# Kernel optimization log

Measured on AMD Instinct MI355X. Metric: run time of the kernel, lower is better.

## Reference

```python
import jax, jax.numpy as jnp
import numpy as np
import math

B, T, DIM = 4, 4096, 1024
HID = int(DIM * 1.5)  # 1536
K = 4                  # conv kernel size
S = 16                 # num_slots
D = 384                # slot_dim


def setup_inputs() -> dict:
    key = jax.random.key(0)
    ks = jax.random.split(key, 16)
    inp = {
        "x": jax.random.normal(ks[0], (B, T, DIM), jnp.float32),
        "input_w": jax.random.normal(ks[1], (2 * HID, DIM), jnp.float32) * DIM ** -0.5,
        "conv_w": jax.random.normal(ks[2], (HID, K), jnp.float32) * K ** -0.5,
        "conv_b": jnp.zeros((HID,), jnp.float32),
        "gates_w": jax.random.normal(ks[3], (2 * HID, HID), jnp.float32) * HID ** -0.5,
        "gates_b": jnp.zeros((2 * HID,), jnp.float32),
        "forget_base": jnp.linspace(-4.323, -9.0, HID).astype(jnp.float32),
        "output_w": jax.random.normal(ks[4], (DIM, HID), jnp.float32) * HID ** -0.5,
        "memory_slots": jax.random.normal(ks[5], (S, D), jnp.float32) * 0.02,
        "wq_w": jax.random.normal(ks[6], (D, D), jnp.float32) * 0.02,
        "wk_w": jax.random.normal(ks[7], (D, HID), jnp.float32) * 0.02,
        "wv_w": jax.random.normal(ks[8], (D, HID), jnp.float32) * 0.02,
        "wg_w": jax.random.normal(ks[9], (1, HID), jnp.float32) * 0.02,
        "rq_w": jax.random.normal(ks[10], (D, HID), jnp.float32) * 0.02,
        "rk_w": jax.random.normal(ks[11], (D, D), jnp.float32) * 0.02,
        "rv_w": jax.random.normal(ks[12], (HID, D), jnp.float32) * 0.02,
    }
    return inp


def _causal_dwconv(x, w, b):
    # x: [B,T,H], w: [H,K], b: [H]; torch Conv1d(padding=K-1) then [:, :T] == causal
    xp = jnp.pad(x, ((0, 0), (K - 1, 0), (0, 0)))
    taps = jnp.stack([xp[:, j:j + T, :] for j in range(K)], axis=-1)  # [B,T,H,K]
    return jnp.einsum('bthk,hk->bth', taps, w) + b


def _scan(alpha, x):
    # h_t = alpha_t * h_{t-1} + x_t, elementwise over channels; along axis 1 (time)
    def combine(c1, c2):
        a1, b1 = c1
        a2, b2 = c2
        return a1 * a2, a2 * b1 + b2
    return jax.lax.associative_scan(combine, (alpha, x), axis=1)[1]


def reference(x, input_w, conv_w, conv_b, gates_w, gates_b, forget_base, output_w,
              memory_slots, wq_w, wk_w, wv_w, wg_w, rq_w, rk_w, rv_w):
    L = T // S  # segment length
    proj = x @ input_w.T                       # [B,T,2H]
    gate, xh = proj[..., :HID], proj[..., HID:]
    xh = _causal_dwconv(xh, conv_w, conv_b)    # [B,T,H]
    g = xh @ gates_w.T + gates_b               # [B,T,2H]
    forget, inp = g[..., :HID], g[..., HID:]
    alpha = jnp.exp(-8.0 * jax.nn.softplus(forget_base) * jax.nn.sigmoid(forget))
    xh = jnp.sqrt(1.0 - alpha ** 2 + 1e-6) * jax.nn.sigmoid(inp) * xh
    h = _scan(alpha, xh)                       # [B,T,H]
    xh = gate * jax.nn.sigmoid(gate) * xh      # silu-gated

    # ---- write_memory(xh) ----
    xseg = xh.reshape(B, S, L, HID)
    q = memory_slots @ wq_w.T                  # [S,D]
    kmat = jnp.einsum('bslh,dh->bsld', xseg, wk_w)
    vmat = jnp.einsum('bslh,dh->bsld', xseg, wv_w)
    qk = jnp.einsum('sd,bsld->bsl', q, kmat) / math.sqrt(D)
    attn = jax.nn.softmax(qk, axis=-1)
    mem = jnp.einsum('bsl,bsld->bsd', attn, vmat)  # [B,S,D]

    # ---- read_memory(gelu(xh)*h, mem) ----
    xr = jax.nn.gelu(xh, approximate=False) * h    # [B,T,H]
    rq = xr @ rq_w.T                               # [B,T,D]
    rk = mem @ rk_w.T                              # [B,S,D]
    rv = mem @ rv_w.T                              # [B,S,H]
    qk2 = jnp.einsum('btd,bsd->bts', rq, rk) / math.sqrt(D)
    seg = jnp.arange(T) // L
    mask = seg[:, None] <= jnp.arange(S)[None, :]  # [T,S]
    qk2 = jnp.where(mask[None], qk2, -jnp.inf)
    attn2 = jax.nn.softmax(qk2, axis=-1)
    out = jnp.einsum('bts,bsh->bth', attn2, rv)
    out = jax.nn.sigmoid(xr @ wg_w.T) * out        # write_gate on xr
    return out @ output_w.T                        # [B,T,DIM]
```

## Files before the change

kernel.cpp:

```cpp
#include <hip/hip_runtime.h>
#include <math.h>

#define BB 4
#define TT 4096
#define DIMW 1024
#define HID 1536
#define HID2 3072
#define KC 4
#define SSEG 16
#define LSEG 256
#define DD 384
#define NCH 64
#define CHL 64
#define TH  ((size_t)TT*(size_t)HID)

typedef _Float16 h8 __attribute__((ext_vector_type(8)));
typedef float f4 __attribute__((ext_vector_type(4)));

#define RSCL 4.8828125e-4f

__device__ __forceinline__ void hsplit(float a, _Float16& h0, _Float16& h1)
{
    _Float16 t = (_Float16)a;
    float tf = (float)t;
    if (fabsf(tf) < 6.103515625e-05f) { t = (_Float16)0.f; tf = 0.f; }
    h0 = t;
    h1 = (_Float16)((a - tf) * 2048.0f);
}

__device__ __forceinline__ void gl_lds16(const _Float16* g, _Float16* l)
{
    __builtin_amdgcn_global_load_lds(
        (const __attribute__((address_space(1))) unsigned int*)g,
        (__attribute__((address_space(3))) unsigned int*)l,
        16, 0, 0);
}

__global__ __launch_bounds__(256) void split2t(const float* __restrict__ src,
                                               _Float16* __restrict__ dst,
                                               int R, int Kd, size_t ps)
{
    __shared__ float tile[64][65];
    const int tid = threadIdx.x;
    const int bx = blockIdx.x;
    const int by = blockIdx.y;
    {
        const int lr = tid >> 2;
        const int lc = (tid & 3) * 16;
        const float* s = src + (size_t)(by * 64 + lr) * Kd + bx * 64 + lc;
#pragma unroll
        for (int e = 0; e < 16; e++) tile[lr][lc + e] = s[e];
    }
    __syncthreads();
    const int c = tid >> 5;
    const int r0 = tid & 31;
#pragma unroll
    for (int rr = 0; rr < 2; rr++) {
        const int r = r0 + rr * 32;
        h8 h0v, h1v;
#pragma unroll
        for (int e = 0; e < 8; e++) {
            _Float16 a0, a1;
            hsplit(tile[r][c * 8 + e], a0, a1);
            h0v[e] = a0; h1v[e] = a1;
        }
        const size_t didx = ((size_t)(bx * 8 + c) * R + by * 64 + r) * 8;
        *(h8*)(dst + didx) = h0v;
        *(h8*)(dst + ps + didx) = h1v;
    }
}

__global__ __launch_bounds__(256) void catkv_kernel(const float* __restrict__ wk,
                                                    const float* __restrict__ wv,
                                                    float* __restrict__ wkv)
{
    const int half = DD * HID;
    int i = blockIdx.x * 256 + threadIdx.x;
    if (i < half) wkv[i] = wk[i];
    else if (i < 2 * half) wkv[i] = wv[i - half];
}

template<int MODE, int TM, int TN, int WRN, int WCN>
__global__ __launch_bounds__(WRN * WCN * 64, 2) void gemm_mfma(
    const _Float16* __restrict__ Ap, size_t aps,
    const _Float16* __restrict__ Wp, size_t wps,
    float* __restrict__ C0, float* __restrict__ C1,
    const float* __restrict__ X,
    _Float16* __restrict__ OP, size_t ops,
    int M, int Nout, int Kd)
{
    constexpr int NWAVE = WRN * WCN;
    constexpr int WTM = TM / WRN, WTN = TN / WCN;
    constexpr int MI = WTM / 16, NI = WTN / 16;
    constexpr int API = TM / 16;
    constexpr int BPI = TN / 16;
    constexpr int ATOT = 2 * API;
    constexpr int NISS = ATOT + 2 * BPI;
    static_assert(NISS % NWAVE == 0, "issue count must divide waves");
    constexpr bool DUAL = (MI * NI <= 16);

    __shared__ _Float16 Als[2][2][TM * 32];
    __shared__ _Float16 Bls[2][2][TN * 32];

    const int tid = threadIdx.x;
    const int lane = tid & 63;
    const int wv = tid >> 6;
    const int wr = wv / WCN, wc = wv % WCN;
    const int lr = lane & 15, lg = lane >> 4;

    int bx = blockIdx.x, by = blockIdx.y;
    {
        const int gx = gridDim.x;
        const int nwg = gx * gridDim.y;
        if ((nwg & 7) == 0) {
            int wg = by * gx + bx;
            wg = (wg & 7) * (nwg >> 3) + (wg >> 3);
            bx = wg % gx; by = wg / gx;
        }
    }
    const int m0 = bx * TM, n0 = by * TN;

    f4 acc1[MI][NI], acc2[MI][NI];
#pragma unroll
    for (int i = 0; i < MI; i++)
#pragma unroll
        for (int j = 0; j < NI; j++) {
            acc1[i][j] = (f4){0.f, 0.f, 0.f, 0.f};
            if constexpr (DUAL) acc2[i][j] = (f4){0.f, 0.f, 0.f, 0.f};
        }

    auto stage = [&](int kq0, int buf) {
#pragma unroll
        for (int j = 0; j < NISS / NWAVE; j++) {
            const int i = j * NWAVE + wv;
            if (i < ATOT) {
                const int pl = i / API, s = i - pl * API;
                const int kc = (s * 64) / TM, r0 = (s * 64) % TM;
                const _Float16* g = Ap + pl * aps
                    + ((size_t)(kq0 + kc) * M + m0 + r0) * 8 + lane * 8;
                gl_lds16(g, &Als[buf][pl][(kc * TM + r0) * 8]);
            } else {
                const int jj = i - ATOT;
                const int pl = jj / BPI, s = jj - pl * BPI;
                const int kc = (s * 64) / TN, r0 = (s * 64) % TN;
                const _Float16* g = Wp + pl * wps
                    + ((size_t)(kq0 + kc) * Nout + n0 + r0) * 8 + lane * 8;
                gl_lds16(g, &Bls[buf][pl][(kc * TN + r0) * 8]);
            }
        }
    };

    stage(0, 0);
    __syncthreads();

    const int NS = Kd / 32;
    for (int t = 0; t < NS; t++) {
        const int buf = t & 1;
        if (t + 1 < NS) stage((t + 1) * 4, buf ^ 1);

        h8 af0[MI], af1[MI];
#pragma unroll
        for (int mi = 0; mi < MI; mi++) {
            const int arow = wr * WTM + mi * 16 + lr;
            af0[mi] = *(const h8*)&Als[buf][0][(lg * TM + arow) * 8];
            af1[mi] = *(const h8*)&Als[buf][1][(lg * TM + arow) * 8];
        }
#pragma unroll
        for (int ni = 0; ni < NI; ni++) {
            const int brow = wc * WTN + ni * 16 + lr;
            h8 b0 = *(const h8*)&Bls[buf][0][(lg * TN + brow) * 8];
            h8 b1 = *(const h8*)&Bls[buf][1][(lg * TN + brow) * 8];
#pragma unroll
            for (int mi = 0; mi < MI; mi++) {
                acc1[mi][ni] = __builtin_amdgcn_mfma_f32_16x16x32_f16(af0[mi], b0, acc1[mi][ni], 0, 0, 0);
                if constexpr (DUAL) {
                    acc2[mi][ni] = __builtin_amdgcn_mfma_f32_16x16x32_f16(af1[mi], b0, acc2[mi][ni], 0, 0, 0);
                    acc2[mi][ni] = __builtin_amdgcn_mfma_f32_16x16x32_f16(af0[mi], b1, acc2[mi][ni], 0, 0, 0);
                } else {
                    f4 tmp = (f4){0.f, 0.f, 0.f, 0.f};
                    tmp = __builtin_amdgcn_mfma_f32_16x16x32_f16(af1[mi], b0, tmp, 0, 0, 0);
                    tmp = __builtin_amdgcn_mfma_f32_16x16x32_f16(af0[mi], b1, tmp, 0, 0, 0);
                    acc1[mi][ni] = acc1[mi][ni] + tmp * RSCL;
                }
            }
        }
        __syncthreads();
    }

#pragma unroll
    for (int mi = 0; mi < MI; mi++) {
#pragma unroll
        for (int ni = 0; ni < NI; ni++) {
#pragma unroll
            for (int r = 0; r < 4; r++) {
                float v;
                if constexpr (DUAL) v = acc1[mi][ni][r] + acc2[mi][ni][r] * RSCL;
                else                v = acc1[mi][ni][r];
                const int m = m0 + wr * WTM + mi * 16 + lg * 4 + r;
                const int n = n0 + wc * WTN + ni * 16 + lr;
                if constexpr (MODE == 1) {
                    if (n < HID) C0[(size_t)m * HID + n] = v;
                    else         C1[(size_t)m * HID + (n - HID)] = v;
                } else if constexpr (MODE == 2) {
                    double g = (double)v;
                    float fv = (float)((g / (1.0 + exp(-g))) * (double)X[(size_t)m * Nout + n]);
                    C0[(size_t)m * Nout + n] = fv;
                    _Float16 a0, a1;
                    hsplit(fv, a0, a1);
                    const size_t didx = ((size_t)(n >> 3) * M + m) * 8 + (n & 7);
                    OP[didx] = a0;
                    OP[ops + didx] = a1;
                } else {
                    C0[(size_t)m * Nout + n] = v;
                }
            }
        }
    }
}

template<int MODE, int TM, int TN>
__global__ __launch_bounds__(256) void gemm32(const float* __restrict__ A,
                                              const float* __restrict__ W,
                                              float* __restrict__ C0,
                                              float* __restrict__ C1,
                                              const float* __restrict__ X,
                                              int M, int Nout, int Kd)
{
    constexpr int GM = TM / 64;
    constexpr int GN = TN / 64;
    constexpr int AF4 = TM * 4;
    constexpr int WF4 = TN * 4;
    constexpr int ALOOP = (AF4 + 255) / 256;
    constexpr int WLOOP = (WF4 + 255) / 256;

    __shared__ float As[16][TM];
    __shared__ float Bs[16][TN];

    const int tid = threadIdx.x;
    const int m0 = blockIdx.x * TM;
    const int n0 = blockIdx.y * TN;
    const int tx = tid & 15, ty = tid >> 4;

    float acc[GM * 4][GN * 4];
#pragma unroll
    for (int i = 0; i < GM * 4; i++)
#pragma unroll
        for (int j = 0; j < GN * 4; j++) acc[i][j] = 0.0f;

    float4 aReg[ALOOP], wReg[WLOOP];

    auto issueLoads = [&](int k0) {
#pragma unroll
        for (int u = 0; u < ALOOP; u++) {
            const int idx = tid + u * 256;
            float4 v = make_float4(0.f, 0.f, 0.f, 0.f);
            if (idx < AF4) {
                const int row = idx >> 2, kq = (idx & 3) * 4;
                const long ar = (long)(m0 + row);
                if (ar < M) v = *(const float4*)(A + ar * (long)Kd + (k0 + kq));
            }
            aReg[u] = v;
        }
#pragma unroll
        for (int u = 0; u < WLOOP; u++) {
            const int idx = tid + u * 256;
            float4 v = make_float4(0.f, 0.f, 0.f, 0.f);
            if (idx < WF4) {
                const int row = idx >> 2, kq = (idx & 3) * 4;
                const long wr = (long)(n0 + row);
                v = *(const float4*)(W + wr * (long)Kd + (k0 + kq));
            }
            wReg[u] = v;
        }
    };
    auto writeLDS = [&]() {
#pragma unroll
        for (int u = 0; u < ALOOP; u++) {
            const int idx = tid + u * 256;
            if (idx < AF4) {
                const int row = idx >> 2, kq = (idx & 3) * 4;
                As[kq + 0][row] = aReg[u].x;
                As[kq + 1][row] = aReg[u].y;
                As[kq + 2][row] = aReg[u].z;
                As[kq + 3][row] = aReg[u].w;
            }
        }
#pragma unroll
        for (int u = 0; u < WLOOP; u++) {
            const int idx = tid + u * 256;
            if (idx < WF4) {
                const int row = idx >> 2, kq = (idx & 3) * 4;
                Bs[kq + 0][row] = wReg[u].x;
                Bs[kq + 1][row] = wReg[u].y;
                Bs[kq + 2][row] = wReg[u].z;
                Bs[kq + 3][row] = wReg[u].w;
            }
        }
    };

    issueLoads(0);
    writeLDS();
    __syncthreads();

    const int NT = Kd / 16;
    for (int t = 0; t < NT; t++) {
        if (t + 1 < NT) issueLoads((t + 1) * 16);
#pragma unroll
        for (int k = 0; k < 16; k++) {
            float a[GM * 4], b[GN * 4];
#pragma unroll
            for (int g = 0; g < GM; g++) {
                const float4 t4 = *(const float4*)&As[k][g * 64 + ty * 4];
                a[g * 4 + 0] = t4.x; a[g * 4 + 1] = t4.y;
                a[g * 4 + 2] = t4.z; a[g * 4 + 3] = t4.w;
            }
#pragma unroll
            for (int g = 0; g < GN; g++) {
                const float4 t4 = *(const float4*)&Bs[k][g * 64 + tx * 4];
                b[g * 4 + 0] = t4.x; b[g * 4 + 1] = t4.y;
                b[g * 4 + 2] = t4.z; b[g * 4 + 3] = t4.w;
            }
#pragma unroll
            for (int i = 0; i < GM * 4; i++)
#pragma unroll
                for (int j = 0; j < GN * 4; j++) acc[i][j] += a[i] * b[j];
        }
        __syncthreads();
        if (t + 1 < NT) {
            writeLDS();
            __syncthreads();
        }
    }

#pragma unroll
    for (int i = 0; i < GM * 4; i++) {
        const int m = m0 + (i >> 2) * 64 + ty * 4 + (i & 3);
        if (m >= M) continue;
#pragma unroll
        for (int j = 0; j < GN * 4; j++) {
            const int n = n0 + (j >> 2) * 64 + tx * 4 + (j & 3);
            if (n >= Nout) continue;
            C0[(long)m * Nout + n] = acc[i][j];
        }
    }
}

__global__ __launch_bounds__(256) void spb_kernel(const float* __restrict__ fb,
                                                  double* __restrict__ spb)
{
    int h = blockIdx.x * 256 + threadIdx.x;
    if (h < HID) {
        double xv = (double)fb[h];
        spb[h] = log1p(exp(xv));
    }
}

__global__ __launch_bounds__(256) void conv_kernel(const float* __restrict__ xin,
                                                   const float* __restrict__ cw,
                                                   const float* __restrict__ cb,
                                                   float* __restrict__ outp,
                                                   _Float16* __restrict__ outP,
                                                   size_t ps)
{
    size_t i = (size_t)blockIdx.x * 256 + threadIdx.x;
    if (i >= TH) return;
    int h = (int)(i % HID);
    int t = (int)(i / HID);
    double acc = (double)cb[h];
#pragma unroll
    for (int j = 0; j < KC; j++) {
        int tt = t - (KC - 1) + j;
        if (tt >= 0) acc += (double)cw[h * KC + j] * (double)xin[(size_t)tt * HID + h];
    }
    float fv = (float)acc;
    outp[i] = fv;
    _Float16 a0, a1;
    hsplit(fv, a0, a1);
    const size_t didx = ((size_t)(h >> 3) * TT + t) * 8 + (h & 7);
    outP[didx] = a0;
    outP[ps + didx] = a1;
}

__global__ __launch_bounds__(256) void alpha_xh2_kernel(float* __restrict__ fg,
                                                        float* __restrict__ ip,
                                                        const float* __restrict__ xh1,
                                                        const double* __restrict__ spb,
                                                        const float* __restrict__ gb)
{
    size_t i = (size_t)blockIdx.x * 256 + threadIdx.x;
    if (i >= TH) return;
    int h = (int)(i % HID);
    double f  = (double)fg[i] + (double)gb[h];
    double g2 = (double)ip[i] + (double)gb[HID + h];
    double sigf = 1.0 / (1.0 + exp(-f));
    double alpha = exp(-8.0 * spb[h] * sigf);
    double s2 = sqrt(1.0 - alpha * alpha + 1e-6);
    double sigi = 1.0 / (1.0 + exp(-g2));
    double x1 = (double)xh1[i];
    fg[i] = (float)alpha;
    ip[i] = (float)(s2 * sigi * x1);
}

__global__ __launch_bounds__(256) void scan1_kernel(const float* __restrict__ alpha,
                                                    const float* __restrict__ xh2,
                                                    double* __restrict__ cA,
                                                    double* __restrict__ cB)
{
    int idx = blockIdx.x * 256 + threadIdx.x;
    if (idx >= NCH * HID) return;
    int h = idx % HID;
    int c = idx / HID;
    size_t base = (size_t)c * CHL * HID + h;
    double aP = 1.0, bV = 0.0;
    for (int i = 0; i < CHL; i++) {
        double a  = (double)alpha[base + (size_t)i * HID];
        double xv = (double)xh2 [base + (size_t)i * HID];
        bV = a * bV + xv;
        aP *= a;
    }
    size_t o = (size_t)c * HID + h;
    cA[o] = aP;
    cB[o] = bV;
}

__global__ __launch_bounds__(256) void scan2_kernel(const double* __restrict__ cA,
                                                    const double* __restrict__ cB,
                                                    double* __restrict__ cH0)
{
    int h = blockIdx.x * 256 + threadIdx.x;
    if (h >= HID) return;
    double carry = 0.0;
    for (int c = 0; c < NCH; c++) {
        size_t o = (size_t)c * HID + h;
        cH0[o] = carry;
        carry = cA[o] * carry + cB[o];
    }
}

__global__ __launch_bounds__(256) void scan3_kernel(const float* __restrict__ alpha,
                                                    const float* __restrict__ xh2,
                                                    const double* __restrict__ cH0,
                                                    float* __restrict__ hout)
{
    int idx = blockIdx.x * 256 + threadIdx.x;
    if (idx >= NCH * HID) return;
    int h = idx % HID;
    int c = idx / HID;
    size_t base = (size_t)c * CHL * HID + h;
    double hv = cH0[(size_t)c * HID + h];
    for (int i = 0; i < CHL; i++) {
        double a  = (double)alpha[base + (size_t)i * HID];
        double xv = (double)xh2 [base + (size_t)i * HID];
        hv = a * hv + xv;
        hout[base + (size_t)i * HID] = (float)hv;
    }
}

__global__ __launch_bounds__(256) void gelu_mul_kernel(float* __restrict__ xh3,
                                                       const float* __restrict__ hbuf,
                                                       _Float16* __restrict__ outP,
                                                       size_t ps)
{
    size_t i = (size_t)blockIdx.x * 256 + threadIdx.x;
    if (i >= TH) return;
    int h = (int)(i % HID);
    int t = (int)(i / HID);
    double x3 = (double)xh3[i];
    double ge = 0.5 * x3 * (1.0 + erf(x3 * 0.70710678118654752440));
    float fv = (float)(ge * (double)hbuf[i]);
    xh3[i] = fv;
    _Float16 a0, a1;
    hsplit(fv, a0, a1);
    const size_t didx = ((size_t)(h >> 3) * TT + t) * 8 + (h & 7);
    outP[didx] = a0;
    outP[ps + didx] = a1;
}

__global__ __launch_bounds__(256) void attn1_kernel(const float* __restrict__ kv,
                                                    const float* __restrict__ qbuf,
                                                    float* __restrict__ mem)
{
    const int s = blockIdx.x;
    const int l = threadIdx.x;
    const size_t row = (size_t)s * LSEG + l;
    const float* kr = kv + row * (2 * DD);
    const float* qs = qbuf + (size_t)s * DD;
    double acc = 0.0;
    for (int d = 0; d < DD; d++) acc += (double)qs[d] * (double)kr[d];
    double qk = acc / sqrt((double)DD);
    __shared__ double r1[256];
    __shared__ double sw[256];
    r1[l] = qk; __syncthreads();
    for (int off = 128; off > 0; off >>= 1) {
        if (l < off) r1[l] = fmax(r1[l], r1[l + off]);
        __syncthreads();
    }
    double m = r1[0]; __syncthreads();
    double e = exp(qk - m);
    r1[l] = e; __syncthreads();
    for (int off = 128; off > 0; off >>= 1) {
        if (l < off) r1[l] += r1[l + off];
        __syncthreads();
    }
    double denom = r1[0];
    sw[l] = e / denom; __syncthreads();
    const size_t vbase = (size_t)s * LSEG * (2 * DD) + DD;
    for (int d = l; d < DD; d += 256) {
        double a2 = 0.0;
        for (int ll = 0; ll < LSEG; ll++)
            a2 += sw[ll] * (double)kv[vbase + (size_t)ll * (2 * DD) + d];
        mem[(size_t)s * DD + d] = (float)a2;
    }
}

__global__ __launch_bounds__(256) void attn2_kernel(const float* __restrict__ rq,
                                                    const float* __restrict__ rk,
                                                    const float* __restrict__ rv,
                                                    const float* __restrict__ xr,
                                                    const float* __restrict__ wg,
                                                    _Float16* __restrict__ outP,
                                                    size_t ps)
{
    const int t = blockIdx.x;
    const int sigma = t >> 8;
    const int tid = threadIdx.x;
    __shared__ double sqk[16];
    __shared__ double red[256];
    __shared__ double sw[16];
    __shared__ double sgate;

    const float* rqn = rq + (size_t)t * DD;
    {
        int s = tid >> 4, j = tid & 15;
        const float* rks = rk + (size_t)s * DD;
        double part = 0.0;
        for (int d = j; d < DD; d += 16) part += (double)rqn[d] * (double)rks[d];
#pragma unroll
        for (int off = 8; off > 0; off >>= 1) part += __shfl_down(part, off, 16);
        if (j == 0) sqk[s] = part;
    }
    double gp = 0.0;
    const float* xrn = xr + (size_t)t * HID;
    for (int hh = tid; hh < HID; hh += 256) gp += (double)xrn[hh] * (double)wg[hh];
    red[tid] = gp; __syncthreads();
    for (int off = 128; off > 0; off >>= 1) {
        if (tid < off) red[tid] += red[tid + off];
        __syncthreads();
    }
    if (tid == 0) {
        const double inv = 1.0 / sqrt((double)DD);
        double m = -1e300;
        for (int ss = sigma; ss < 16; ss++) {
            double v = sqk[ss] * inv;
            sqk[ss] = v;
            if (v > m) m = v;
        }
        double sum = 0.0;
        for (int ss = sigma; ss < 16; ss++) {
            double e = exp(sqk[ss] - m);
            sw[ss] = e;
            sum += e;
        }
        double isum = 1.0 / sum;
        for (int ss = 0; ss < sigma; ss++) sw[ss] = 0.0;
        for (int ss = sigma; ss < 16; ss++) sw[ss] *= isum;
        sgate = 1.0 / (1.0 + exp(-red[0]));
    }
    __syncthreads();
    const double gte = sgate;
    for (int c = tid; c < HID / 8; c += 256) {
        double accv[8] = {0, 0, 0, 0, 0, 0, 0, 0};
        for (int ss = sigma; ss < 16; ss++) {
            const float* rvp = rv + (size_t)ss * HID + c * 8;
            double w = sw[ss];
#pragma unroll
            for (int e = 0; e < 8; e++) accv[e] += w * (double)rvp[e];
        }
        h8 h0v, h1v;
#pragma unroll
        for (int e = 0; e < 8; e++) {
            _Float16 a0, a1;
            hsplit((float)(gte * accv[e]), a0, a1);
            h0v[e] = a0; h1v[e] = a1;
        }
        const size_t didx = ((size_t)c * TT + t) * 8;
        *(h8*)(outP + didx) = h0v;
        *(h8*)(outP + ps + didx) = h1v;
    }
}

extern "C" void kernel_launch(void* const* d_in, const int* in_sizes, int n_in,
                              void* d_out, int out_size, void* d_ws, size_t ws_size,
                              hipStream_t stream)
{
    const float* x            = (const float*)d_in[0];
    const float* input_w      = (const float*)d_in[1];
    const float* conv_w       = (const float*)d_in[2];
    const float* conv_b       = (const float*)d_in[3];
    const float* gates_w      = (const float*)d_in[4];
    const float* gates_b      = (const float*)d_in[5];
    const float* forget_base  = (const float*)d_in[6];
    const float* output_w     = (const float*)d_in[7];
    const float* memory_slots = (const float*)d_in[8];
    const float* wq_w         = (const float*)d_in[9];
    const float* wk_w         = (const float*)d_in[10];
    const float* wv_w         = (const float*)d_in[11];
    const float* wg_w         = (const float*)d_in[12];
    const float* rq_w         = (const float*)d_in[13];
    const float* rk_w         = (const float*)d_in[14];
    const float* rv_w         = (const float*)d_in[15];
    float* out = (float*)d_out;

    double* spb  = (double*)d_ws;
    double* cA   = spb + HID;
    double* cB   = cA + (size_t)NCH * HID;
    double* cH0  = cB + (size_t)NCH * HID;
    float* slotA = (float*)(cH0 + (size_t)NCH * HID);
    float* slotB = slotA + TH;
    float* slotC = slotB + TH;
    float* qbuf   = slotC + TH;
    float* membuf = qbuf + (size_t)SSEG * DD;
    float* rkbuf  = membuf + (size_t)SSEG * DD;
    float* rvbuf  = rkbuf + (size_t)SSEG * DD;

    _Float16* base_h = (_Float16*)(rvbuf + (size_t)SSEG * HID);
    const size_t iwN  = (size_t)HID * DIMW;
    const size_t gwN  = (size_t)HID2 * HID;
    const size_t kvN  = (size_t)(2 * DD) * HID;
    const size_t rqN  = (size_t)DD * HID;
    const size_t owN  = (size_t)DIMW * HID;
    const size_t xbN  = (size_t)TT * DIMW;
    _Float16* iwlo = base_h;
    _Float16* iwhi = iwlo + 2 * iwN;
    _Float16* gwp  = iwhi + 2 * iwN;
    _Float16* wkvp = gwp  + 2 * gwN;
    _Float16* rqwp = wkvp + 2 * kvN;
    _Float16* owp  = rqwp + 2 * rqN;
    _Float16* xbP  = owp  + 2 * owN;
    _Float16* P1   = xbP  + 2 * xbN;

    dim3 blk(256);
    dim3 blk512(512);
    const int ewBlocks = (int)(TH / 256);

    spb_kernel<<<(HID + 255) / 256, blk, 0, stream>>>(forget_base, spb);
    catkv_kernel<<<(2 * DD * HID) / 256, blk, 0, stream>>>(wk_w, wv_w, slotA);
    split2t<<<dim3(DIMW / 64, HID / 64), blk, 0, stream>>>(input_w, iwlo, HID, DIMW, iwN);
    split2t<<<dim3(DIMW / 64, HID / 64), blk, 0, stream>>>(input_w + (size_t)HID * DIMW,
                                                           iwhi, HID, DIMW, iwN);
    split2t<<<dim3(HID / 64, HID2 / 64), blk, 0, stream>>>(gates_w, gwp, HID2, HID, gwN);
    split2t<<<dim3(HID / 64, (2 * DD) / 64), blk, 0, stream>>>(slotA, wkvp, 2 * DD, HID, kvN);
    split2t<<<dim3(HID / 64, DD / 64), blk, 0, stream>>>(rq_w, rqwp, DD, HID, rqN);
    split2t<<<dim3(HID / 64, DIMW / 64), blk, 0, stream>>>(output_w, owp, DIMW, HID, owN);
    gemm32<0, 64, 64><<<dim3(1, DD / 64), blk, 0, stream>>>(
        memory_slots, wq_w, qbuf, (float*)nullptr, (const float*)nullptr, SSEG, DD, DD);

    for (int b = 0; b < BB; b++) {
        const float* xb   = x   + (size_t)b * TT * DIMW;
        float*       outb = out + (size_t)b * TT * DIMW;

        split2t<<<dim3(DIMW / 64, TT / 64), blk, 0, stream>>>(xb, xbP, TT, DIMW, xbN);
        gemm_mfma<0, 256, 128, 4, 2><<<dim3(TT / 256, HID / 128), blk512, 0, stream>>>(
            xbP, xbN, iwhi, iwN, slotB, (float*)nullptr, (const float*)nullptr,
            (_Float16*)nullptr, 0, TT, HID, DIMW);
        conv_kernel<<<ewBlocks, blk, 0, stream>>>(slotB, conv_w, conv_b, slotC, P1, TH);
        gemm_mfma<1, 256, 256, 4, 2><<<dim3(TT / 256, HID2 / 256), blk512, 0, stream>>>(
            P1, TH, gwp, gwN, slotA, slotB, (const float*)nullptr,
            (_Float16*)nullptr, 0, TT, HID2, HID);
        alpha_xh2_kernel<<<ewBlocks, blk, 0, stream>>>(slotA, slotB, slotC, spb, gates_b);
        scan1_kernel<<<(NCH * HID) / 256, blk, 0, stream>>>(slotA, slotB, cA, cB);
        scan2_kernel<<<(HID + 255) / 256, blk, 0, stream>>>(cA, cB, cH0);
        scan3_kernel<<<(NCH * HID) / 256, blk, 0, stream>>>(slotA, slotB, cH0, slotC);
        gemm_mfma<2, 256, 128, 4, 2><<<dim3(TT / 256, HID / 128), blk512, 0, stream>>>(
            xbP, xbN, iwlo, iwN, slotA, (float*)nullptr, slotB, P1, TH, TT, HID, DIMW);
        gemm_mfma<0, 128, 128, 2, 2><<<dim3(TT / 128, (2 * DD) / 128), blk, 0, stream>>>(
            P1, TH, wkvp, kvN, slotB, (float*)nullptr, (const float*)nullptr,
            (_Float16*)nullptr, 0, TT, 2 * DD, HID);
        attn1_kernel<<<SSEG, blk, 0, stream>>>(slotB, qbuf, membuf);
        gelu_mul_kernel<<<ewBlocks, blk, 0, stream>>>(slotA, slotC, P1, TH);
        gemm_mfma<0, 128, 128, 2, 2><<<dim3(TT / 128, DD / 128), blk, 0, stream>>>(
            P1, TH, rqwp, rqN, slotB, (float*)nullptr, (const float*)nullptr,
            (_Float16*)nullptr, 0, TT, DD, HID);
        gemm32<0, 64, 64><<<dim3(1, DD / 64), blk, 0, stream>>>(
            membuf, rk_w, rkbuf, (float*)nullptr, (const float*)nullptr, SSEG, DD, DD);
        gemm32<0, 64, 64><<<dim3(1, HID / 64), blk, 0, stream>>>(
            membuf, rv_w, rvbuf, (float*)nullptr, (const float*)nullptr, SSEG, HID, DD);
        attn2_kernel<<<TT, blk, 0, stream>>>(slotB, rkbuf, rvbuf, slotA, wg_w, P1, TH);
        gemm_mfma<0, 128, 128, 2, 2><<<dim3(TT / 128, DIMW / 128), blk, 0, stream>>>(
            P1, TH, owp, owN, outb, (float*)nullptr, (const float*)nullptr,
            (_Float16*)nullptr, 0, TT, DIMW, HID);
    }
}
```

Baseline: 2.736 ms.

## Fuse forget-gate alpha into gates GEMM, move elementwise math to fp32, retile GEMMs

The forget-gate sigmoid and alpha exponent now run in the gates GEMM epilogue instead of a separate elementwise pass. Several elementwise kernels (conv, silu, gelu, xh2) switch from double to float math, which cuts slow FP64 work. The large GEMMs move from 256-wide 512-thread tiles to 128x128 256-thread tiles, and rk/rv are merged into one concatenated small GEMM. The fp32 math and the smaller tiles could shift accuracy and raise memory traffic, respectively.

Measured after the change: 2.659 ms. 1.03x faster.

```diff
diff --git a/kernel.cpp b/kernel.cpp
--- a/kernel.cpp
+++ b/kernel.cpp
@@ -13,6 +13,7 @@
 #define NCH 64
 #define CHL 64
 #define TH  ((size_t)TT*(size_t)HID)
+#define RKVN (DD + HID)
 
 typedef _Float16 h8 __attribute__((ext_vector_type(8)));
 typedef float f4 __attribute__((ext_vector_type(4)));
@@ -70,14 +71,13 @@
     }
 }
 
-__global__ __launch_bounds__(256) void catkv_kernel(const float* __restrict__ wk,
-                                                    const float* __restrict__ wv,
-                                                    float* __restrict__ wkv)
-{
-    const int half = DD * HID;
+__global__ __launch_bounds__(256) void ccat2_kernel(const float* __restrict__ s1, int n1,
+                                                    const float* __restrict__ s2, int n2,
+                                                    float* __restrict__ dst)
+{
     int i = blockIdx.x * 256 + threadIdx.x;
-    if (i < half) wkv[i] = wk[i];
-    else if (i < 2 * half) wkv[i] = wv[i - half];
+    if (i < n1) dst[i] = s1[i];
+    else if (i < n1 + n2) dst[i] = s2[i - n1];
 }
 
 template<int MODE, int TM, int TN, int WRN, int WCN>
@@ -87,6 +87,7 @@
     float* __restrict__ C0, float* __restrict__ C1,
     const float* __restrict__ X,
     _Float16* __restrict__ OP, size_t ops,
+    const double* __restrict__ SPB, const float* __restrict__ GB,
     int M, int Nout, int Kd)
 {
     constexpr int NWAVE = WRN * WCN;
@@ -97,7 +98,7 @@
     constexpr int ATOT = 2 * API;
     constexpr int NISS = ATOT + 2 * BPI;
     static_assert(NISS % NWAVE == 0, "issue count must divide waves");
-    constexpr bool DUAL = (MI * NI <= 16);
+    static_assert(MI * NI <= 16, "DUAL only");
 
     __shared__ _Float16 Als[2][2][TM * 32];
     __shared__ _Float16 Bls[2][2][TN * 32];
@@ -126,7 +127,7 @@
 #pragma unroll
         for (int j = 0; j < NI; j++) {
             acc1[i][j] = (f4){0.f, 0.f, 0.f, 0.f};
-            if constexpr (DUAL) acc2[i][j] = (f4){0.f, 0.f, 0.f, 0.f};
+            acc2[i][j] = (f4){0.f, 0.f, 0.f, 0.f};
         }
 
     auto stage = [&](int kq0, int buf) {
@@ -136,16 +137,14 @@
             if (i < ATOT) {
                 const int pl = i / API, s = i - pl * API;
                 const int kc = (s * 64) / TM, r0 = (s * 64) % TM;
-                const _Float16* g = Ap + pl * aps
-                    + ((size_t)(kq0 + kc) * M + m0 + r0) * 8 + lane * 8;
-                gl_lds16(g, &Als[buf][pl][(kc * TM + r0) * 8]);
+                gl_lds16(Ap + pl * aps + ((size_t)(kq0 + kc) * M + m0 + r0) * 8 + lane * 8,
+                         &Als[buf][pl][(kc * TM + r0) * 8]);
             } else {
                 const int jj = i - ATOT;
                 const int pl = jj / BPI, s = jj - pl * BPI;
                 const int kc = (s * 64) / TN, r0 = (s * 64) % TN;
-                const _Float16* g = Wp + pl * wps
-                    + ((size_t)(kq0 + kc) * Nout + n0 + r0) * 8 + lane * 8;
-                gl_lds16(g, &Bls[buf][pl][(kc * TN + r0) * 8]);
+                gl_lds16(Wp + pl * wps + ((size_t)(kq0 + kc) * Nout + n0 + r0) * 8 + lane * 8,
+                         &Bls[buf][pl][(kc * TN + r0) * 8]);
             }
         }
     };
@@ -173,15 +172,8 @@
 #pragma unroll
             for (int mi = 0; mi < MI; mi++) {
                 acc1[mi][ni] = __builtin_amdgcn_mfma_f32_16x16x32_f16(af0[mi], b0, acc1[mi][ni], 0, 0, 0);
-                if constexpr (DUAL) {
-                    acc2[mi][ni] = __builtin_amdgcn_mfma_f32_16x16x32_f16(af1[mi], b0, acc2[mi][ni], 0, 0, 0);
-                    acc2[mi][ni] = __builtin_amdgcn_mfma_f32_16x16x32_f16(af0[mi], b1, acc2[mi][ni], 0, 0, 0);
-                } else {
-                    f4 tmp = (f4){0.f, 0.f, 0.f, 0.f};
-                    tmp = __builtin_amdgcn_mfma_f32_16x16x32_f16(af1[mi], b0, tmp, 0, 0, 0);
-                    tmp = __builtin_amdgcn_mfma_f32_16x16x32_f16(af0[mi], b1, tmp, 0, 0, 0);
-                    acc1[mi][ni] = acc1[mi][ni] + tmp * RSCL;
-                }
+                acc2[mi][ni] = __builtin_amdgcn_mfma_f32_16x16x32_f16(af1[mi], b0, acc2[mi][ni], 0, 0, 0);
+                acc2[mi][ni] = __builtin_amdgcn_mfma_f32_16x16x32_f16(af0[mi], b1, acc2[mi][ni], 0, 0, 0);
             }
         }
         __syncthreads();
@@ -193,17 +185,20 @@
         for (int ni = 0; ni < NI; ni++) {
 #pragma unroll
             for (int r = 0; r < 4; r++) {
-                float v;
-                if constexpr (DUAL) v = acc1[mi][ni][r] + acc2[mi][ni][r] * RSCL;
-                else                v = acc1[mi][ni][r];
+                const float v = acc1[mi][ni][r] + acc2[mi][ni][r] * RSCL;
                 const int m = m0 + wr * WTM + mi * 16 + lg * 4 + r;
                 const int n = n0 + wc * WTN + ni * 16 + lr;
-                if constexpr (MODE == 1) {
-                    if (n < HID) C0[(size_t)m * HID + n] = v;
-                    else         C1[(size_t)m * HID + (n - HID)] = v;
+                if constexpr (MODE == 3) {
+                    if (n < HID) {
+                        double f = (double)v + (double)GB[n];
+                        double sigf = 1.0 / (1.0 + exp(-f));
+                        C0[(size_t)m * HID + n] = (float)exp(-8.0 * SPB[n] * sigf);
+                    } else {
+                        C1[(size_t)m * HID + (n - HID)] = v;
+                    }
                 } else if constexpr (MODE == 2) {
-                    double g = (double)v;
-                    float fv = (float)((g / (1.0 + exp(-g))) * (double)X[(size_t)m * Nout + n]);
+                    float g = v;
+                    float fv = (g / (1.0f + expf(-g))) * X[(size_t)m * Nout + n];
                     C0[(size_t)m * Nout + n] = fv;
                     _Float16 a0, a1;
                     hsplit(fv, a0, a1);
@@ -218,12 +213,10 @@
     }
 }
 
-template<int MODE, int TM, int TN>
+template<int TM, int TN>
 __global__ __launch_bounds__(256) void gemm32(const float* __restrict__ A,
                                               const float* __restrict__ W,
                                               float* __restrict__ C0,
-                                              float* __restrict__ C1,
-                                              const float* __restrict__ X,
                                               int M, int Nout, int Kd)
 {
     constexpr int GM = TM / 64;
@@ -268,7 +261,7 @@
             if (idx < WF4) {
                 const int row = idx >> 2, kq = (idx & 3) * 4;
                 const long wr = (long)(n0 + row);
-                v = *(const float4*)(W + wr * (long)Kd + (k0 + kq));
+                if (wr < Nout) v = *(const float4*)(W + wr * (long)Kd + (k0 + kq));
             }
             wReg[u] = v;
         }
@@ -366,39 +359,33 @@
     if (i >= TH) return;
     int h = (int)(i % HID);
     int t = (int)(i / HID);
-    double acc = (double)cb[h];
+    float acc = cb[h];
 #pragma unroll
     for (int j = 0; j < KC; j++) {
         int tt = t - (KC - 1) + j;
-        if (tt >= 0) acc += (double)cw[h * KC + j] * (double)xin[(size_t)tt * HID + h];
-    }
-    float fv = (float)acc;
-    outp[i] = fv;
+        if (tt >= 0) acc = fmaf(cw[h * KC + j], xin[(size_t)tt * HID + h], acc);
+    }
+    outp[i] = acc;
     _Float16 a0, a1;
-    hsplit(fv, a0, a1);
+    hsplit(acc, a0, a1);
     const size_t didx = ((size_t)(h >> 3) * TT + t) * 8 + (h & 7);
     outP[didx] = a0;
     outP[ps + didx] = a1;
 }
 
-__global__ __launch_bounds__(256) void alpha_xh2_kernel(float* __restrict__ fg,
-                                                        float* __restrict__ ip,
-                                                        const float* __restrict__ xh1,
-                                                        const double* __restrict__ spb,
-                                                        const float* __restrict__ gb)
+__global__ __launch_bounds__(256) void xh2_kernel(const float* __restrict__ alpha,
+                                                  float* __restrict__ ip,
+                                                  const float* __restrict__ xh1,
+                                                  const float* __restrict__ gb)
 {
     size_t i = (size_t)blockIdx.x * 256 + threadIdx.x;
     if (i >= TH) return;
     int h = (int)(i % HID);
-    double f  = (double)fg[i] + (double)gb[h];
-    double g2 = (double)ip[i] + (double)gb[HID + h];
-    double sigf = 1.0 / (1.0 + exp(-f));
-    double alpha = exp(-8.0 * spb[h] * sigf);
-    double s2 = sqrt(1.0 - alpha * alpha + 1e-6);
-    double sigi = 1.0 / (1.0 + exp(-g2));
-    double x1 = (double)xh1[i];
-    fg[i] = (float)alpha;
-    ip[i] = (float)(s2 * sigi * x1);
+    float a = alpha[i];
+    float g2 = ip[i] + gb[HID + h];
+    float s2 = sqrtf(1.0f - a * a + 1e-6f);
+    float sigi = 1.0f / (1.0f + expf(-g2));
+    ip[i] = s2 * sigi * xh1[i];
 }
 
 __global__ __launch_bounds__(256) void scan1_kernel(const float* __restrict__ alpha,
@@ -465,9 +452,9 @@
     if (i >= TH) return;
     int h = (int)(i % HID);
     int t = (int)(i / HID);
-    double x3 = (double)xh3[i];
-    double ge = 0.5 * x3 * (1.0 + erf(x3 * 0.70710678118654752440));
-    float fv = (float)(ge * (double)hbuf[i]);
+    float x3 = xh3[i];
+    float ge = 0.5f * x3 * (1.0f + erff(x3 * 0.70710678f));
+    float fv = ge * hbuf[i];
     xh3[i] = fv;
     _Float16 a0, a1;
     hsplit(fv, a0, a1);
@@ -514,8 +501,7 @@
 }
 
 __global__ __launch_bounds__(256) void attn2_kernel(const float* __restrict__ rq,
-                                                    const float* __restrict__ rk,
-                                                    const float* __restrict__ rv,
+                                                    const float* __restrict__ rkv,
                                                     const float* __restrict__ xr,
                                                     const float* __restrict__ wg,
                                                     _Float16* __restrict__ outP,
@@ -532,7 +518,7 @@
     const float* rqn = rq + (size_t)t * DD;
     {
         int s = tid >> 4, j = tid & 15;
-        const float* rks = rk + (size_t)s * DD;
+        const float* rks = rkv + (size_t)s * RKVN;
         double part = 0.0;
         for (int d = j; d < DD; d += 16) part += (double)rqn[d] * (double)rks[d];
 #pragma unroll
@@ -571,7 +557,7 @@
     for (int c = tid; c < HID / 8; c += 256) {
         double accv[8] = {0, 0, 0, 0, 0, 0, 0, 0};
         for (int ss = sigma; ss < 16; ss++) {
-            const float* rvp = rv + (size_t)ss * HID + c * 8;
+            const float* rvp = rkv + (size_t)ss * RKVN + DD + c * 8;
             double w = sw[ss];
 #pragma unroll
             for (int e = 0; e < 8; e++) accv[e] += w * (double)rvp[e];
@@ -620,10 +606,10 @@
     float* slotC = slotB + TH;
     float* qbuf   = slotC + TH;
     float* membuf = qbuf + (size_t)SSEG * DD;
-    float* rkbuf  = membuf + (size_t)SSEG * DD;
-    float* rvbuf  = rkbuf + (size_t)SSEG * DD;
-
-    _Float16* base_h = (_Float16*)(rvbuf + (size_t)SSEG * HID);
+    float* rkvw   = membuf + (size_t)SSEG * DD;
+    float* rkvbuf = rkvw + (size_t)RKVN * DD;
+
+    _Float16* base_h = (_Float16*)(rkvbuf + (size_t)SSEG * RKVN);
     const size_t iwN  = (size_t)HID * DIMW;
     const size_t gwN  = (size_t)HID2 * HID;
     const size_t kvN  = (size_t)(2 * DD) * HID;
@@ -640,11 +626,13 @@
     _Float16* P1   = xbP  + 2 * xbN;
 
     dim3 blk(256);
-    dim3 blk512(512);
     const int ewBlocks = (int)(TH / 256);
 
     spb_kernel<<<(HID + 255) / 256, blk, 0, stream>>>(forget_base, spb);
-    catkv_kernel<<<(2 * DD * HID) / 256, blk, 0, stream>>>(wk_w, wv_w, slotA);
+    ccat2_kernel<<<(2 * DD * HID + 255) / 256, blk, 0, stream>>>(
+        wk_w, DD * HID, wv_w, DD * HID, slotA);
+    ccat2_kernel<<<(RKVN * DD + 255) / 256, blk, 0, stream>>>(
+        rk_w, DD * DD, rv_w, HID * DD, rkvw);
     split2t<<<dim3(DIMW / 64, HID / 64), blk, 0, stream>>>(input_w, iwlo, HID, DIMW, iwN);
     split2t<<<dim3(DIMW / 64, HID / 64), blk, 0, stream>>>(input_w + (size_t)HID * DIMW,
                                                            iwhi, HID, DIMW, iwN);
@@ -652,42 +640,45 @@
     split2t<<<dim3(HID / 64, (2 * DD) / 64), blk, 0, stream>>>(slotA, wkvp, 2 * DD, HID, kvN);
     split2t<<<dim3(HID / 64, DD / 64), blk, 0, stream>>>(rq_w, rqwp, DD, HID, rqN);
     split2t<<<dim3(HID / 64, DIMW / 64), blk, 0, stream>>>(output_w, owp, DIMW, HID, owN);
-    gemm32<0, 64, 64><<<dim3(1, DD / 64), blk, 0, stream>>>(
-        memory_slots, wq_w, qbuf, (float*)nullptr, (const float*)nullptr, SSEG, DD, DD);
+    gemm32<64, 64><<<dim3(1, DD / 64), blk, 0, stream>>>(
+        memory_slots, wq_w, qbuf, SSEG, DD, DD);
 
     for (int b = 0; b < BB; b++) {
         const float* xb   = x   + (size_t)b * TT * DIMW;
         float*       outb = out + (size_t)b * TT * DIMW;
 
         split2t<<<dim3(DIMW / 64, TT / 64), blk, 0, stream>>>(xb, xbP, TT, DIMW, xbN);
-        gemm_mfma<0, 256, 128, 4, 2><<<dim3(TT / 256, HID / 128), blk512, 0, stream>>>(
+        gemm_mfma<0, 128, 128, 2, 2><<<dim3(TT / 128, HID / 128), blk, 0, stream>>>(
             xbP, xbN, iwhi, iwN, slotB, (float*)nullptr, (const float*)nullptr,
-            (_Float16*)nullptr, 0, TT, HID, DIMW);
+            (_Float16*)nullptr, 0, (const double*)nullptr, (const float*)nullptr,
+            TT, HID, DIMW);
         conv_kernel<<<ewBlocks, blk, 0, stream>>>(slotB, conv_w, conv_b, slotC, P1, TH);
-        gemm_mfma<1, 256, 256, 4, 2><<<dim3(TT / 256, HID2 / 256), blk512, 0, stream>>>(
+        gemm_mfma<3, 128, 128, 2, 2><<<dim3(TT / 128, HID2 / 128), blk, 0, stream>>>(
             P1, TH, gwp, gwN, slotA, slotB, (const float*)nullptr,
-            (_Float16*)nullptr, 0, TT, HID2, HID);
-        alpha_xh2_kernel<<<ewBlocks, blk, 0, stream>>>(slotA, slotB, slotC, spb, gates_b);
+            (_Float16*)nullptr, 0, spb, gates_b, TT, HID2, HID);
+        xh2_kernel<<<ewBlocks, blk, 0, stream>>>(slotA, slotB, slotC, gates_b);
         scan1_kernel<<<(NCH * HID) / 256, blk, 0, stream>>>(slotA, slotB, cA, cB);
         scan2_kernel<<<(HID + 255) / 256, blk, 0, stream>>>(cA, cB, cH0);
         scan3_kernel<<<(NCH * HID) / 256, blk, 0, stream>>>(slotA, slotB, cH0, slotC);
-        gemm_mfma<2, 256, 128, 4, 2><<<dim3(TT / 256, HID / 128), blk512, 0, stream>>>(
-            xbP, xbN, iwlo, iwN, slotA, (float*)nullptr, slotB, P1, TH, TT, HID, DIMW);
+        gemm_mfma<2, 128, 128, 2, 2><<<dim3(TT / 128, HID / 128), blk, 0, stream>>>(
+            xbP, xbN, iwlo, iwN, slotA, (float*)nullptr, slotB, P1, TH,
+            (const double*)nullptr, (const float*)nullptr, TT, HID, DIMW);
         gemm_mfma<0, 128, 128, 2, 2><<<dim3(TT / 128, (2 * DD) / 128), blk, 0, stream>>>(
             P1, TH, wkvp, kvN, slotB, (float*)nullptr, (const float*)nullptr,
-            (_Float16*)nullptr, 0, TT, 2 * DD, HID);
+            (_Float16*)nullptr, 0, (const double*)nullptr, (const float*)nullptr,
+            TT, 2 * DD, HID);
         attn1_kernel<<<SSEG, blk, 0, stream>>>(slotB, qbuf, membuf);
         gelu_mul_kernel<<<ewBlocks, blk, 0, stream>>>(slotA, slotC, P1, TH);
-        gemm_mfma<0, 128, 128, 2, 2><<<dim3(TT / 128, DD / 128), blk, 0, stream>>>(
+        gemm_mfma<0, 64, 128, 2, 2><<<dim3(TT / 64, DD / 128), blk, 0, stream>>>(
             P1, TH, rqwp, rqN, slotB, (float*)nullptr, (const float*)nullptr,
-            (_Float16*)nullptr, 0, TT, DD, HID);
-        gemm32<0, 64, 64><<<dim3(1, DD / 64), blk, 0, stream>>>(
-            membuf, rk_w, rkbuf, (float*)nullptr, (const float*)nullptr, SSEG, DD, DD);
-        gemm32<0, 64, 64><<<dim3(1, HID / 64), blk, 0, stream>>>(
-            membuf, rv_w, rvbuf, (float*)nullptr, (const float*)nullptr, SSEG, HID, DD);
-        attn2_kernel<<<TT, blk, 0, stream>>>(slotB, rkbuf, rvbuf, slotA, wg_w, P1, TH);
+            (_Float16*)nullptr, 0, (const double*)nullptr, (const float*)nullptr,
+            TT, DD, HID);
+        gemm32<64, 64><<<dim3(1, (RKVN + 63) / 64), blk, 0, stream>>>(
+            membuf, rkvw, rkvbuf, SSEG, RKVN, DD);
+        attn2_kernel<<<TT, blk, 0, stream>>>(slotB, rkvbuf, slotA, wg_w, P1, TH);
         gemm_mfma<0, 128, 128, 2, 2><<<dim3(TT / 128, DIMW / 128), blk, 0, stream>>>(
             P1, TH, owp, owN, outb, (float*)nullptr, (const float*)nullptr,
-            (_Float16*)nullptr, 0, TT, DIMW, HID);
-    }
-}
+            (_Float16*)nullptr, 0, (const double*)nullptr, (const float*)nullptr,
+            TT, DIMW, HID);
+    }
+}
```
